# Optimization experiments

Measured on AMD Instinct MI355X. Metric: run time of the kernel, lower is better.

The kernel has to match this reference:

```python
import jax, jax.numpy as jnp
import numpy as np

NEG_BIG = -9e15
ALPHA = 0.2  # leaky relu slope

def setup_inputs() -> dict:
    key = jax.random.key(0)
    k1, k2, k3, k4, k5 = jax.random.split(key, 5)
    N, F_in, F_out, H = 4096, 512, 64, 8
    x = jax.random.normal(k1, (N, F_in), dtype=jnp.float32)
    adj = jax.random.randint(k2, (N, N), 0, 2, dtype=jnp.int32)
    W = jax.random.normal(k3, (H, F_in, F_out), dtype=jnp.float32) * (1.414 * (2.0 / (F_in + F_out)) ** 0.5)
    a_source = jax.random.normal(k4, (H, 1, F_out), dtype=jnp.float32) * (1.414 * (2.0 / (1 + F_out)) ** 0.5)
    a_target = jax.random.normal(k5, (H, 1, F_out), dtype=jnp.float32) * (1.414 * (2.0 / (1 + F_out)) ** 0.5)
    return {"x": x, "adj": adj, "W": W, "a_source": a_source, "a_target": a_target}

def reference(x, adj, W, a_source, a_target):
    # Wh: [H, N, F_out]
    Wh = jnp.einsum('nf,hfo->hno', x, W)
    # additive attention logits
    s_i = jnp.sum(a_source * Wh, axis=2, keepdims=True)          # [H, N, 1]
    s_j = jnp.sum(a_target * Wh, axis=2, keepdims=True)          # [H, N, 1]
    e = s_i + jnp.swapaxes(s_j, 1, 2)                            # [H, N, N]
    e = jnp.where(e > 0, e, ALPHA * e)                           # leaky relu
    e = jnp.where(adj[None] > 0, e, jnp.float32(NEG_BIG))        # adjacency mask
    attention = jax.nn.softmax(e, axis=2)                        # [H, N, N]
    h_prime = jnp.einsum('hij,hjo->hio', attention, Wh)          # [H, N, F_out]
    return h_prime
```

## Files before the change

kernel.cpp:

```cpp
#include <hip/hip_runtime.h>
#include <hip/hip_fp16.h>
#include <cstdint>

#define N_NODES 4096
#define F_IN    512
#define F_OUT   64
#define H_HEADS 8
#define JC      4

constexpr float L2E = 1.44269504088896f;

typedef _Float16 half2_t __attribute__((ext_vector_type(2)));
typedef _Float16 half4_t __attribute__((ext_vector_type(4)));
typedef _Float16 half8_t __attribute__((ext_vector_type(8)));
typedef float    f32x4   __attribute__((ext_vector_type(4)));

__device__ inline unsigned int exp2_pk_u(unsigned int au) {
    __half2 h = __builtin_bit_cast(__half2, au);
    h = h2exp2(h);
    return __builtin_bit_cast(unsigned int, h);
}

__global__ __launch_bounds__(256) void k_prep(const int* __restrict__ adj,
                                              const float* __restrict__ W,
                                              unsigned long long* __restrict__ adjwT,
                                              _Float16* __restrict__ wfrag) {
    if (blockIdx.x < 128) {
        int gid = blockIdx.x * 256 + threadIdx.x;
        int h     = gid >> 12;
        int kt    = (gid >> 8) & 15;
        int ntile = (gid >> 6) & 3;
        int lane  = gid & 63;
        int c0 = lane & 15, g = lane >> 4;
        const float* src = W + ((size_t)h * F_IN + kt * 32 + 8 * g) * F_OUT + ntile * 16 + c0;
        half8_t hv;
        #pragma unroll
        for (int t = 0; t < 8; t++) hv[t] = (_Float16)src[(size_t)t * F_OUT];
        *reinterpret_cast<half8_t*>(&wfrag[(size_t)gid * 8]) = hv;
        return;
    }
    int bid  = blockIdx.x - 128;
    int lane = threadIdx.x & 63;
    int wid  = (int)((bid * 256 + threadIdx.x) >> 6);
    int nwaves = (2048 * 256) >> 6;
    const int nchunks = N_NODES * (N_NODES / 64);
    for (int cf = wid; cf < nchunks; cf += nwaves) {
        int v = adj[(size_t)cf * 64 + lane];
        unsigned long long mask = __ballot(v > 0);
        if (lane == 0) {
            int i = cf >> 6, c = cf & 63;
            adjwT[(size_t)c * N_NODES + i] = mask;
        }
    }
}

__global__ __launch_bounds__(512) void k_wh_mfma(const float* __restrict__ x,
                                                 const _Float16* __restrict__ wfrag,
                                                 const float* __restrict__ a_src,
                                                 const float* __restrict__ a_tgt,
                                                 _Float16* __restrict__ WhFrag,
                                                 float* __restrict__ s_iL,
                                                 _Float16* __restrict__ s_jLh) {
    __shared__ f32x4 red[4][4][64];
    const int h    = blockIdx.y;
    const int rt   = blockIdx.x;
    const int t    = threadIdx.x;
    const int lane = t & 63;
    const int w    = t >> 6;
    const int mtw  = w & 3;
    const int kh   = w >> 2;
    const int mt   = rt * 4 + mtw;
    const int c0   = lane & 15;
    const int gl   = lane >> 4;

    f32x4 acc0 = {0.f, 0.f, 0.f, 0.f};
    f32x4 acc1 = {0.f, 0.f, 0.f, 0.f};
    f32x4 acc2 = {0.f, 0.f, 0.f, 0.f};
    f32x4 acc3 = {0.f, 0.f, 0.f, 0.f};

    const float* __restrict__ xr = x + (size_t)(mt * 16 + c0) * F_IN + 8 * gl + kh * 256;
    const _Float16* __restrict__ Bf = wfrag + (size_t)h * (16 * 4 * 512)
                                    + (size_t)kh * 8 * 2048 + (size_t)lane * 8;

    #pragma unroll
    for (int kt = 0; kt < 8; kt++) {
        float4 v0 = *reinterpret_cast<const float4*>(xr + kt * 32);
        float4 v1 = *reinterpret_cast<const float4*>(xr + kt * 32 + 4);
        half8_t a;
        a[0] = (_Float16)v0.x; a[1] = (_Float16)v0.y; a[2] = (_Float16)v0.z; a[3] = (_Float16)v0.w;
        a[4] = (_Float16)v1.x; a[5] = (_Float16)v1.y; a[6] = (_Float16)v1.z; a[7] = (_Float16)v1.w;
        const _Float16* Bk = Bf + (size_t)kt * 2048;
        half8_t b0 = *reinterpret_cast<const half8_t*>(Bk);
        half8_t b1 = *reinterpret_cast<const half8_t*>(Bk + 512);
        half8_t b2 = *reinterpret_cast<const half8_t*>(Bk + 1024);
        half8_t b3 = *reinterpret_cast<const half8_t*>(Bk + 1536);
        acc0 = __builtin_amdgcn_mfma_f32_16x16x32_f16(a, b0, acc0, 0, 0, 0);
        acc1 = __builtin_amdgcn_mfma_f32_16x16x32_f16(a, b1, acc1, 0, 0, 0);
        acc2 = __builtin_amdgcn_mfma_f32_16x16x32_f16(a, b2, acc2, 0, 0, 0);
        acc3 = __builtin_amdgcn_mfma_f32_16x16x32_f16(a, b3, acc3, 0, 0, 0);
    }

    if (kh == 1) {
        red[mtw][0][lane] = acc0;
        red[mtw][1][lane] = acc1;
        red[mtw][2][lane] = acc2;
        red[mtw][3][lane] = acc3;
    }
    __syncthreads();
    if (kh == 1) return;

    acc0 += red[mtw][0][lane];
    acc1 += red[mtw][1][lane];
    acc2 += red[mtw][2][lane];
    acc3 += red[mtw][3][lane];

    const float as0 = a_src[h * 64 + c0],      at0 = a_tgt[h * 64 + c0];
    const float as1 = a_src[h * 64 + 16 + c0], at1 = a_tgt[h * 64 + 16 + c0];
    const float as2 = a_src[h * 64 + 32 + c0], at2 = a_tgt[h * 64 + 32 + c0];
    const float as3 = a_src[h * 64 + 48 + c0], at3 = a_tgt[h * 64 + 48 + c0];

    #pragma unroll
    for (int reg = 0; reg < 4; reg++) {
        float vi = acc0[reg] * as0 + acc1[reg] * as1 + acc2[reg] * as2 + acc3[reg] * as3;
        float vj = acc0[reg] * at0 + acc1[reg] * at1 + acc2[reg] * at2 + acc3[reg] * at3;
        #pragma unroll
        for (int mm = 8; mm >= 1; mm >>= 1) {
            vi += __shfl_xor(vi, mm, 64);
            vj += __shfl_xor(vj, mm, 64);
        }
        if (c0 == 0) {
            int row = mt * 16 + 4 * gl + reg;
            s_iL[h * N_NODES + row]  = vi * L2E;
            s_jLh[h * N_NODES + row] = (_Float16)(vj * L2E);
        }
    }

    const int cc    = mt >> 2;
    const int kb    = (mt >> 1) & 1;
    const int lanep = c0 + 16 * ((mt & 1) * 2 + (gl >> 1));
    const int tb    = 4 * (gl & 1);
    _Float16* dst = WhFrag + (size_t)h * (N_NODES * 64)
                  + (size_t)(cc * 2 + kb) * 2048 + (size_t)lanep * 8 + tb;
    f32x4 accs[4] = {acc0, acc1, acc2, acc3};
    #pragma unroll
    for (int ot = 0; ot < 4; ot++) {
        half4_t hv;
        #pragma unroll
        for (int reg = 0; reg < 4; reg++) hv[reg] = (_Float16)accs[ot][reg];
        *reinterpret_cast<half4_t*>(dst + ot * 512) = hv;
    }
}

__global__ __launch_bounds__(256) void k_hmax(const _Float16* __restrict__ s_jLh,
                                              float* __restrict__ mxAll) {
    __shared__ float red[4];
    const int h = blockIdx.x;
    const int t = threadIdx.x;
    const _Float16* p = s_jLh + h * N_NODES;
    float m = -INFINITY;
    for (int k = t; k < N_NODES; k += 256) m = fmaxf(m, (float)p[k]);
    #pragma unroll
    for (int mm = 32; mm >= 1; mm >>= 1) m = fmaxf(m, __shfl_xor(m, mm, 64));
    if ((t & 63) == 0) red[t >> 6] = m;
    __syncthreads();
    if (t == 0) mxAll[h] = fmaxf(fmaxf(red[0], red[1]), fmaxf(red[2], red[3]));
}

__global__ __launch_bounds__(256, 4) void k_attn_mfma(const _Float16* __restrict__ WhFrag,
                                                      const float* __restrict__ s_iL,
                                                      const float* __restrict__ mxAll,
                                                      const _Float16* __restrict__ s_jLh,
                                                      const unsigned long long* __restrict__ adjwT,
                                                      float* __restrict__ out0,
                                                      _Float16* __restrict__ partH,
                                                      float* __restrict__ lbuf) {
    __shared__ unsigned int ktab[256][4];
    __shared__ _Float16 Bs[2][8192];
    {
        unsigned int bm = threadIdx.x;
        #pragma unroll
        for (int q = 0; q < 4; q++) {
            unsigned int lo = ((bm >> (2 * q)) & 1u) ? 0xFFFFu : 0u;
            unsigned int hi = ((bm >> (2 * q + 1)) & 1u) ? 0xFFFF0000u : 0u;
            ktab[bm][q] = lo | hi;
        }
    }

    const int tid  = threadIdx.x;
    const int h    = blockIdx.y;
    const int jc   = blockIdx.z;
    const int lane = tid & 63;
    const int w    = tid >> 6;
    const int i0   = blockIdx.x * 128 + w * 32;
    const int mrow = lane & 15;
    const int gl   = lane >> 4;
    const int gl8  = gl << 3;

    const float siL0 = s_iL[h * N_NODES + i0 + mrow];
    const float siL1 = s_iL[h * N_NODES + i0 + 16 + mrow];
    const float mxh  = mxAll[h];
    const float tm0 = siL0 + mxh, tm1 = siL1 + mxh;
    const float m0 = fmaxf(tm0, 0.2f * tm0);
    const float m1 = fmaxf(tm1, 0.2f * tm1);
    const half2_t u2_0 = {(_Float16)(siL0 - m0), (_Float16)(siL0 - m0)};
    const half2_t u2_1 = {(_Float16)(siL1 - m1), (_Float16)(siL1 - m1)};
    const half2_t n82_0 = {(_Float16)(-0.8f * m0), (_Float16)(-0.8f * m0)};
    const half2_t n82_1 = {(_Float16)(-0.8f * m1), (_Float16)(-0.8f * m1)};
    const half2_t c02 = {(_Float16)0.2f, (_Float16)0.2f};

    const _Float16* __restrict__ sjh = s_jLh + h * N_NODES;
    const _Float16* __restrict__ Bh  = WhFrag + (size_t)h * (N_NODES * 64);

    half8_t vone;
    #pragma unroll
    for (int q = 0; q < 8; q++) vone[q] = (_Float16)1.0f;

    f32x4 accA0 = {0,0,0,0}, accA1 = {0,0,0,0}, accA2 = {0,0,0,0}, accA3 = {0,0,0,0};
    f32x4 accB0 = {0,0,0,0}, accB1 = {0,0,0,0}, accB2 = {0,0,0,0}, accB3 = {0,0,0,0};
    f32x4 acclA = {0,0,0,0}, acclB = {0,0,0,0};

    const int NC   = (N_NODES / 64) / JC;
    const int cbeg = jc * NC;
    const int cend = cbeg + NC;

    {
        #pragma unroll
        for (int s = 0; s < 4; s++)
            *reinterpret_cast<half8_t*>(&Bs[0][s * 2048 + tid * 8]) =
                *reinterpret_cast<const half8_t*>(Bh + (size_t)cbeg * 4096 + s * 2048 + tid * 8);
    }
    __syncthreads();

    int cur = 0;
    for (int cp = cbeg; cp < cend; cp += 2) {
        half8_t nx0, nx1, nx2, nx3;
        const bool hasNext = (cp + 2 < cend);
        if (hasNext) {
            const _Float16* src = Bh + (size_t)(cp + 2) * 4096 + tid * 8;
            nx0 = *reinterpret_cast<const half8_t*>(src);
            nx1 = *reinterpret_cast<const half8_t*>(src + 2048);
            nx2 = *reinterpret_cast<const half8_t*>(src + 4096);
            nx3 = *reinterpret_cast<const half8_t*>(src + 6144);
        }

        #pragma unroll
        for (int ci = 0; ci < 2; ci++) {
            const int c = cp + ci;
            uint2 word0 = *reinterpret_cast<const uint2*>(&adjwT[(size_t)c * N_NODES + i0 + mrow]);
            uint2 word1 = *reinterpret_cast<const uint2*>(&adjwT[(size_t)c * N_NODES + i0 + 16 + mrow]);

            #pragma unroll
            for (int kb = 0; kb < 2; kb++) {
                const int jb = c * 64 + kb * 32 + 8 * gl;
                half8_t sjv = *reinterpret_cast<const half8_t*>(&sjh[jb]);
                unsigned int bm0 = ((kb ? word0.y : word0.x) >> gl8) & 0xFFu;
                unsigned int bm1 = ((kb ? word1.y : word1.x) >> gl8) & 0xFFu;
                uint4 mk0 = *reinterpret_cast<const uint4*>(&ktab[bm0][0]);
                uint4 mk1 = *reinterpret_cast<const uint4*>(&ktab[bm1][0]);

                uint4 sju = __builtin_bit_cast(uint4, sjv);
                uint4 p0u, p1u;
                #pragma unroll
                for (int q = 0; q < 4; q++) {
                    unsigned int sw = (q == 0) ? sju.x : (q == 1) ? sju.y : (q == 2) ? sju.z : sju.w;
                    half2_t sj2 = __builtin_bit_cast(half2_t, sw);
                    half2_t a1 = u2_0 + sj2;
                    half2_t am = __builtin_elementwise_max(a1, a1 * c02 + n82_0);
                    unsigned int pa = exp2_pk_u(__builtin_bit_cast(unsigned int, am));
                    half2_t b1 = u2_1 + sj2;
                    half2_t bmv = __builtin_elementwise_max(b1, b1 * c02 + n82_1);
                    unsigned int pb = exp2_pk_u(__builtin_bit_cast(unsigned int, bmv));
                    unsigned int ka  = (q == 0) ? mk0.x : (q == 1) ? mk0.y : (q == 2) ? mk0.z : mk0.w;
                    unsigned int kbm = (q == 0) ? mk1.x : (q == 1) ? mk1.y : (q == 2) ? mk1.z : mk1.w;
                    pa &= ka; pb &= kbm;
                    if (q == 0) { p0u.x = pa; p1u.x = pb; }
                    else if (q == 1) { p0u.y = pa; p1u.y = pb; }
                    else if (q == 2) { p0u.z = pa; p1u.z = pb; }
                    else { p0u.w = pa; p1u.w = pb; }
                }
                half8_t af0 = __builtin_bit_cast(half8_t, p0u);
                half8_t af1 = __builtin_bit_cast(half8_t, p1u);

                const _Float16* Bk = &Bs[cur][ci * 4096 + kb * 2048 + lane * 8];
                half8_t b0  = *reinterpret_cast<const half8_t*>(Bk);
                half8_t b1v = *reinterpret_cast<const half8_t*>(Bk + 512);
                half8_t b2  = *reinterpret_cast<const half8_t*>(Bk + 1024);
                half8_t b3  = *reinterpret_cast<const half8_t*>(Bk + 1536);

                accA0 = __builtin_amdgcn_mfma_f32_16x16x32_f16(af0, b0,  accA0, 0, 0, 0);
                accB0 = __builtin_amdgcn_mfma_f32_16x16x32_f16(af1, b0,  accB0, 0, 0, 0);
                accA1 = __builtin_amdgcn_mfma_f32_16x16x32_f16(af0, b1v, accA1, 0, 0, 0);
                accB1 = __builtin_amdgcn_mfma_f32_16x16x32_f16(af1, b1v, accB1, 0, 0, 0);
                accA2 = __builtin_amdgcn_mfma_f32_16x16x32_f16(af0, b2,  accA2, 0, 0, 0);
                accB2 = __builtin_amdgcn_mfma_f32_16x16x32_f16(af1, b2,  accB2, 0, 0, 0);
                accA3 = __builtin_amdgcn_mfma_f32_16x16x32_f16(af0, b3,  accA3, 0, 0, 0);
                accB3 = __builtin_amdgcn_mfma_f32_16x16x32_f16(af1, b3,  accB3, 0, 0, 0);
                acclA = __builtin_amdgcn_mfma_f32_16x16x32_f16(af0, vone, acclA, 0, 0, 0);
                acclB = __builtin_amdgcn_mfma_f32_16x16x32_f16(af1, vone, acclB, 0, 0, 0);
            }
        }

        if (hasNext) {
            *reinterpret_cast<half8_t*>(&Bs[cur ^ 1][tid * 8])        = nx0;
            *reinterpret_cast<half8_t*>(&Bs[cur ^ 1][2048 + tid * 8]) = nx1;
            *reinterpret_cast<half8_t*>(&Bs[cur ^ 1][4096 + tid * 8]) = nx2;
            *reinterpret_cast<half8_t*>(&Bs[cur ^ 1][6144 + tid * 8]) = nx3;
        }
        __syncthreads();
        cur ^= 1;
    }

    float* lp = lbuf + (size_t)jc * (H_HEADS * N_NODES);
    if (mrow == 0) {
        #pragma unroll
        for (int r = 0; r < 4; r++) {
            lp[h * N_NODES + i0 + 4 * gl + r]      = acclA[r];
            lp[h * N_NODES + i0 + 16 + 4 * gl + r] = acclB[r];
        }
    }
    if (jc == 0) {
        #pragma unroll
        for (int r = 0; r < 4; r++) {
            size_t obA = ((size_t)h * N_NODES + i0 + 4 * gl + r) * 64 + mrow;
            size_t obB = ((size_t)h * N_NODES + i0 + 16 + 4 * gl + r) * 64 + mrow;
            out0[obA + 0]  = accA0[r];
            out0[obA + 16] = accA1[r];
            out0[obA + 32] = accA2[r];
            out0[obA + 48] = accA3[r];
            out0[obB + 0]  = accB0[r];
            out0[obB + 16] = accB1[r];
            out0[obB + 32] = accB2[r];
            out0[obB + 48] = accB3[r];
        }
    } else {
        _Float16* op = partH + (size_t)(jc - 1) * ((size_t)H_HEADS * N_NODES * F_OUT);
        #pragma unroll
        for (int r = 0; r < 4; r++) {
            size_t obA = ((size_t)h * N_NODES + i0 + 4 * gl + r) * 64 + mrow;
            size_t obB = ((size_t)h * N_NODES + i0 + 16 + 4 * gl + r) * 64 + mrow;
            op[obA + 0]  = (_Float16)accA0[r];
            op[obA + 16] = (_Float16)accA1[r];
            op[obA + 32] = (_Float16)accA2[r];
            op[obA + 48] = (_Float16)accA3[r];
            op[obB + 0]  = (_Float16)accB0[r];
            op[obB + 16] = (_Float16)accB1[r];
            op[obB + 32] = (_Float16)accB2[r];
            op[obB + 48] = (_Float16)accB3[r];
        }
    }
}

__global__ __launch_bounds__(256) void k_norm(float* __restrict__ out,
                                              const _Float16* __restrict__ partH,
                                              const float* __restrict__ lbuf) {
    const int HN = H_HEADS * N_NODES;
    int idx = blockIdx.x * 256 + threadIdx.x;
    int row = idx >> 4;
    float inv = 1.0f / (lbuf[row] + lbuf[HN + row] + lbuf[2 * HN + row] + lbuf[3 * HN + row]);
    float4 a = reinterpret_cast<const float4*>(out)[idx];
    float s0 = a.x, s1 = a.y, s2 = a.z, s3 = a.w;
    #pragma unroll
    for (int p = 0; p < 3; p++) {
        half4_t hp = *reinterpret_cast<const half4_t*>(
            &partH[(size_t)p * ((size_t)H_HEADS * N_NODES * F_OUT) + (size_t)idx * 4]);
        s0 += (float)hp[0]; s1 += (float)hp[1]; s2 += (float)hp[2]; s3 += (float)hp[3];
    }
    float4 v = {s0 * inv, s1 * inv, s2 * inv, s3 * inv};
    reinterpret_cast<float4*>(out)[idx] = v;
}

extern "C" void kernel_launch(void* const* d_in, const int* in_sizes, int n_in,
                              void* d_out, int out_size, void* d_ws, size_t ws_size,
                              hipStream_t stream) {
    const float* x     = (const float*)d_in[0];
    const int*   adj   = (const int*)d_in[1];
    const float* W     = (const float*)d_in[2];
    const float* a_src = (const float*)d_in[3];
    const float* a_tgt = (const float*)d_in[4];
    float* out = (float*)d_out;

    char* ws = (char*)d_ws;
    size_t off = 0;
    auto alloc = [&](size_t bytes) -> char* {
        char* p = ws + off;
        off += (bytes + 255) & ~(size_t)255;
        return p;
    };
    _Float16* WhFrag = (_Float16*)alloc((size_t)H_HEADS * N_NODES * F_OUT * 2);
    _Float16* wfrag  = (_Float16*)alloc((size_t)H_HEADS * 16 * 4 * 64 * 8 * 2);
    float* s_iL      = (float*)alloc((size_t)H_HEADS * N_NODES * 4);
    _Float16* s_jLh  = (_Float16*)alloc((size_t)H_HEADS * N_NODES * 2);
    float* mxAll     = (float*)alloc((size_t)H_HEADS * 4);
    float* lbuf      = (float*)alloc((size_t)JC * H_HEADS * N_NODES * 4);
    _Float16* partH  = (_Float16*)alloc((size_t)(JC - 1) * H_HEADS * N_NODES * F_OUT * 2);
    unsigned long long* adjwT = (unsigned long long*)alloc((size_t)N_NODES * (N_NODES / 64) * 8);
    (void)ws_size;

    k_prep<<<2176, 256, 0, stream>>>(adj, W, adjwT, wfrag);
    k_wh_mfma<<<dim3(N_NODES / 64, H_HEADS), 512, 0, stream>>>(x, wfrag, a_src, a_tgt,
                                                               WhFrag, s_iL, s_jLh);
    k_hmax<<<H_HEADS, 256, 0, stream>>>(s_jLh, mxAll);
    k_attn_mfma<<<dim3(N_NODES / 128, H_HEADS, JC), 256, 0, stream>>>(WhFrag, s_iL, mxAll, s_jLh,
                                                                      adjwT, out, partH, lbuf);
    k_norm<<<(H_HEADS * N_NODES * F_OUT / 4) / 256, 256, 0, stream>>>(out, partH, lbuf);
}
```

Baseline: 80.21 us.

## Pre-pack x to fp16 fragments and fuse head max into Wh kernel

Adds a k_xpack kernel that converts x to fp16 in MFMA fragment layout once, so k_wh_mfma no longer re-reads and converts fp32 x for every head. Removes the separate k_hmax kernel by computing the per-head max of s_j inside k_wh_mfma with an order-preserving uint encoding and atomicMax, which needs a memset. This trades one small launch for another plus a memset, and adds atomic contention on 8 addresses. The max is now taken over the fp32 values rather than the fp16-rounded ones.

```diff
diff --git a/kernel.cpp b/kernel.cpp
--- a/kernel.cpp
+++ b/kernel.cpp
@@ -19,6 +19,15 @@
     __half2 h = __builtin_bit_cast(__half2, au);
     h = h2exp2(h);
     return __builtin_bit_cast(unsigned int, h);
+}
+
+__device__ inline unsigned int fenc(float x) {
+    unsigned int u = __float_as_uint(x);
+    return (u & 0x80000000u) ? ~u : (u | 0x80000000u);
+}
+__device__ inline float fdec(unsigned int e) {
+    unsigned int u = (e & 0x80000000u) ? (e ^ 0x80000000u) : ~e;
+    return __uint_as_float(u);
 }
 
 __global__ __launch_bounds__(256) void k_prep(const int* __restrict__ adj,
@@ -54,13 +63,30 @@
     }
 }
 
-__global__ __launch_bounds__(512) void k_wh_mfma(const float* __restrict__ x,
+__global__ __launch_bounds__(256) void k_xpack(const float* __restrict__ x,
+                                               _Float16* __restrict__ xfrag) {
+    int gid = blockIdx.x * 256 + threadIdx.x;
+    int kt   = gid >> 14;
+    int mt   = (gid >> 6) & 255;
+    int lane = gid & 63;
+    int r = lane & 15, g = lane >> 4;
+    const float* src = x + (size_t)(mt * 16 + r) * F_IN + kt * 32 + 8 * g;
+    float4 v0 = *reinterpret_cast<const float4*>(src);
+    float4 v1 = *reinterpret_cast<const float4*>(src + 4);
+    half8_t hv;
+    hv[0] = (_Float16)v0.x; hv[1] = (_Float16)v0.y; hv[2] = (_Float16)v0.z; hv[3] = (_Float16)v0.w;
+    hv[4] = (_Float16)v1.x; hv[5] = (_Float16)v1.y; hv[6] = (_Float16)v1.z; hv[7] = (_Float16)v1.w;
+    *reinterpret_cast<half8_t*>(&xfrag[(size_t)gid * 8]) = hv;
+}
+
+__global__ __launch_bounds__(512) void k_wh_mfma(const _Float16* __restrict__ xfrag,
                                                  const _Float16* __restrict__ wfrag,
                                                  const float* __restrict__ a_src,
                                                  const float* __restrict__ a_tgt,
                                                  _Float16* __restrict__ WhFrag,
                                                  float* __restrict__ s_iL,
-                                                 _Float16* __restrict__ s_jLh) {
+                                                 _Float16* __restrict__ s_jLh,
+                                                 unsigned int* __restrict__ mxEnc) {
     __shared__ f32x4 red[4][4][64];
     const int h    = blockIdx.y;
     const int rt   = blockIdx.x;
@@ -78,17 +104,14 @@
     f32x4 acc2 = {0.f, 0.f, 0.f, 0.f};
     f32x4 acc3 = {0.f, 0.f, 0.f, 0.f};
 
-    const float* __restrict__ xr = x + (size_t)(mt * 16 + c0) * F_IN + 8 * gl + kh * 256;
+    const _Float16* __restrict__ Af = xfrag + (size_t)(kh * 8) * (256 * 512)
+                                    + (size_t)mt * 512 + (size_t)lane * 8;
     const _Float16* __restrict__ Bf = wfrag + (size_t)h * (16 * 4 * 512)
                                     + (size_t)kh * 8 * 2048 + (size_t)lane * 8;
 
     #pragma unroll
     for (int kt = 0; kt < 8; kt++) {
-        float4 v0 = *reinterpret_cast<const float4*>(xr + kt * 32);
-        float4 v1 = *reinterpret_cast<const float4*>(xr + kt * 32 + 4);
-        half8_t a;
-        a[0] = (_Float16)v0.x; a[1] = (_Float16)v0.y; a[2] = (_Float16)v0.z; a[3] = (_Float16)v0.w;
-        a[4] = (_Float16)v1.x; a[5] = (_Float16)v1.y; a[6] = (_Float16)v1.z; a[7] = (_Float16)v1.w;
+        half8_t a = *reinterpret_cast<const half8_t*>(Af + (size_t)kt * (256 * 512));
         const _Float16* Bk = Bf + (size_t)kt * 2048;
         half8_t b0 = *reinterpret_cast<const half8_t*>(Bk);
         half8_t b1 = *reinterpret_cast<const half8_t*>(Bk + 512);
@@ -119,6 +142,7 @@
     const float as2 = a_src[h * 64 + 32 + c0], at2 = a_tgt[h * 64 + 32 + c0];
     const float as3 = a_src[h * 64 + 48 + c0], at3 = a_tgt[h * 64 + 48 + c0];
 
+    float sjmax = -INFINITY;
     #pragma unroll
     for (int reg = 0; reg < 4; reg++) {
         float vi = acc0[reg] * as0 + acc1[reg] * as1 + acc2[reg] * as2 + acc3[reg] * as3;
@@ -128,12 +152,17 @@
             vi += __shfl_xor(vi, mm, 64);
             vj += __shfl_xor(vj, mm, 64);
         }
+        float sjl = vj * L2E;
+        sjmax = fmaxf(sjmax, sjl);
         if (c0 == 0) {
             int row = mt * 16 + 4 * gl + reg;
             s_iL[h * N_NODES + row]  = vi * L2E;
-            s_jLh[h * N_NODES + row] = (_Float16)(vj * L2E);
-        }
-    }
+            s_jLh[h * N_NODES + row] = (_Float16)sjl;
+        }
+    }
+    sjmax = fmaxf(sjmax, __shfl_xor(sjmax, 16, 64));
+    sjmax = fmaxf(sjmax, __shfl_xor(sjmax, 32, 64));
+    if (lane == 0) atomicMax(&mxEnc[h], fenc(sjmax));
 
     const int cc    = mt >> 2;
     const int kb    = (mt >> 1) & 1;
@@ -151,24 +180,9 @@
     }
 }
 
-__global__ __launch_bounds__(256) void k_hmax(const _Float16* __restrict__ s_jLh,
-                                              float* __restrict__ mxAll) {
-    __shared__ float red[4];
-    const int h = blockIdx.x;
-    const int t = threadIdx.x;
-    const _Float16* p = s_jLh + h * N_NODES;
-    float m = -INFINITY;
-    for (int k = t; k < N_NODES; k += 256) m = fmaxf(m, (float)p[k]);
-    #pragma unroll
-    for (int mm = 32; mm >= 1; mm >>= 1) m = fmaxf(m, __shfl_xor(m, mm, 64));
-    if ((t & 63) == 0) red[t >> 6] = m;
-    __syncthreads();
-    if (t == 0) mxAll[h] = fmaxf(fmaxf(red[0], red[1]), fmaxf(red[2], red[3]));
-}
-
 __global__ __launch_bounds__(256, 4) void k_attn_mfma(const _Float16* __restrict__ WhFrag,
                                                       const float* __restrict__ s_iL,
-                                                      const float* __restrict__ mxAll,
+                                                      const unsigned int* __restrict__ mxEnc,
                                                       const _Float16* __restrict__ s_jLh,
                                                       const unsigned long long* __restrict__ adjwT,
                                                       float* __restrict__ out0,
@@ -198,7 +212,7 @@
 
     const float siL0 = s_iL[h * N_NODES + i0 + mrow];
     const float siL1 = s_iL[h * N_NODES + i0 + 16 + mrow];
-    const float mxh  = mxAll[h];
+    const float mxh  = fdec(mxEnc[h]);
     const float tm0 = siL0 + mxh, tm1 = siL1 + mxh;
     const float m0 = fmaxf(tm0, 0.2f * tm0);
     const float m1 = fmaxf(tm1, 0.2f * tm1);
@@ -387,20 +401,23 @@
         return p;
     };
     _Float16* WhFrag = (_Float16*)alloc((size_t)H_HEADS * N_NODES * F_OUT * 2);
+    _Float16* xfrag  = (_Float16*)alloc((size_t)N_NODES * F_IN * 2);
     _Float16* wfrag  = (_Float16*)alloc((size_t)H_HEADS * 16 * 4 * 64 * 8 * 2);
     float* s_iL      = (float*)alloc((size_t)H_HEADS * N_NODES * 4);
     _Float16* s_jLh  = (_Float16*)alloc((size_t)H_HEADS * N_NODES * 2);
-    float* mxAll     = (float*)alloc((size_t)H_HEADS * 4);
+    unsigned int* mxEnc = (unsigned int*)alloc((size_t)H_HEADS * 4);
     float* lbuf      = (float*)alloc((size_t)JC * H_HEADS * N_NODES * 4);
     _Float16* partH  = (_Float16*)alloc((size_t)(JC - 1) * H_HEADS * N_NODES * F_OUT * 2);
     unsigned long long* adjwT = (unsigned long long*)alloc((size_t)N_NODES * (N_NODES / 64) * 8);
     (void)ws_size;
 
+    hipMemsetAsync(mxEnc, 0, H_HEADS * 4, stream);
+
     k_prep<<<2176, 256, 0, stream>>>(adj, W, adjwT, wfrag);
-    k_wh_mfma<<<dim3(N_NODES / 64, H_HEADS), 512, 0, stream>>>(x, wfrag, a_src, a_tgt,
-                                                               WhFrag, s_iL, s_jLh);
-    k_hmax<<<H_HEADS, 256, 0, stream>>>(s_jLh, mxAll);
-    k_attn_mfma<<<dim3(N_NODES / 128, H_HEADS, JC), 256, 0, stream>>>(WhFrag, s_iL, mxAll, s_jLh,
+    k_xpack<<<1024, 256, 0, stream>>>(x, xfrag);
+    k_wh_mfma<<<dim3(N_NODES / 64, H_HEADS), 512, 0, stream>>>(xfrag, wfrag, a_src, a_tgt,
+                                                               WhFrag, s_iL, s_jLh, mxEnc);
+    k_attn_mfma<<<dim3(N_NODES / 128, H_HEADS, JC), 256, 0, stream>>>(WhFrag, s_iL, mxEnc, s_jLh,
                                                                       adjwT, out, partH, lbuf);
     k_norm<<<(H_HEADS * N_NODES * F_OUT / 4) / 256, 256, 0, stream>>>(out, partH, lbuf);
 }
```

Result: slower. 101.2 us (+26.2%).
